# Kernel tuning notes

Measured on AMD Instinct MI355X. Metric: run time of the kernel, lower is better.

The kernel has to match this reference:

```python
import jax, jax.numpy as jnp
import numpy as np

N_NODES = 100000
N_EDGES = 1600000
NFEAT, NHID, NCLASS = 256, 128, 64


def gcn_conv(x, edge_index, edge_weight, W):
    # PyG GCNConv (normalize=False, add_self_loops=False, bias=False):
    # h = x @ W.T; out[i] = sum over edges (j->i) of w_e * h[j]
    h = x @ W.T                                   # [N, out]
    src, dst = edge_index[0], edge_index[1]
    msgs = h[src] * edge_weight[:, None]          # [E, out]
    return jax.ops.segment_sum(msgs, dst, num_segments=x.shape[0])


def setup_inputs() -> dict:
    key = jax.random.key(0)
    ks = jax.random.split(key, 7)
    x = jax.random.normal(ks[0], (N_NODES, NFEAT), dtype=jnp.float32)
    edge_index1 = jax.random.randint(ks[1], (2, N_EDGES), 0, N_NODES, dtype=jnp.int64)
    edge_index2 = jax.random.randint(ks[2], (2, N_EDGES), 0, N_NODES, dtype=jnp.int64)
    edge_weight1 = jax.random.uniform(ks[3], (N_EDGES,), dtype=jnp.float32)
    edge_weight2 = jax.random.uniform(ks[4], (N_EDGES,), dtype=jnp.float32)
    W1 = jax.random.normal(ks[5], (NHID, NFEAT), dtype=jnp.float32) * (1.0 / np.sqrt(NFEAT))
    W2 = jax.random.normal(ks[6], (NCLASS, NHID), dtype=jnp.float32) * (1.0 / np.sqrt(NHID))
    return {"x": x, "edge_index1": edge_index1, "edge_index2": edge_index2,
            "edge_weight1": edge_weight1, "edge_weight2": edge_weight2,
            "W1": W1, "W2": W2}


def reference(x, edge_index1, edge_index2, edge_weight1, edge_weight2, W1, W2):
    h = jax.nn.relu(gcn_conv(x, edge_index1, edge_weight1, W1))
    out = gcn_conv(h, edge_index2, edge_weight2, W2)
    return out
```

## Files before the change

kernel.cpp:

```cpp
#include <hip/hip_runtime.h>

typedef __attribute__((ext_vector_type(8))) short short8;
typedef __attribute__((ext_vector_type(4))) float floatx4;

#define BKT_SHIFT 8
#define BKT_MASK 255
#define SORT_CAP 6144

__device__ __forceinline__ ushort f2bf(float f) {
    uint u = __builtin_bit_cast(uint, f);
    uint r = (u + 0x7FFFu + ((u >> 16) & 1u)) >> 16;
    return (ushort)r;
}
__device__ __forceinline__ float bf2f(ushort u) {
    return __builtin_bit_cast(float, (uint)u << 16);
}

__global__ void detect_i64(const uint* __restrict__ p, int* __restrict__ flag) {
    uint v = p[2 * threadIdx.x + 1];
    unsigned long long b = __ballot(v != 0u);
    if (threadIdx.x == 0) *flag = (b == 0ull) ? 1 : 0;
}

__global__ __launch_bounds__(256) void cvt_w(const float* __restrict__ W1,
                                             const float* __restrict__ W2,
                                             ushort* __restrict__ w1b,
                                             ushort* __restrict__ w2b, int n1, int n2) {
    int i = blockIdx.x * 256 + threadIdx.x;
    if (i < n1) w1b[i] = f2bf(W1[i]);
    else if (i < n1 + n2) w2b[i - n1] = f2bf(W2[i - n1]);
}

template<int K, int NOUT, bool XF32>
__global__ __launch_bounds__(256) void gemm_bt(const void* __restrict__ Xv,
                                               const ushort* __restrict__ W,
                                               ushort* __restrict__ Y, int N) {
    constexpr int NT = NOUT / 16;
    constexpr int KS = K / 32;
    constexpr int ROWS = 64;
    constexpr int RB = XF32 ? K * 4 : K * 2;
    __shared__ __align__(16) char xs[ROWS * RB];

    const int tid  = threadIdx.x;
    const int lane = tid & 63;
    const int wv   = tid >> 6;
    const int t    = lane & 15;
    const int q    = lane >> 4;
    const int rbase = blockIdx.x * ROWS;

    if (XF32) {
        #pragma unroll
        for (int i = 0; i < 16; i++) {
            int rl = wv * 16 + i;
            int grow = rbase + rl;
            if (grow < N) {
                const char* src = (const char*)Xv + (long)grow * RB
                                + ((lane * 16) ^ ((rl & 7) << 5));
                __builtin_amdgcn_global_load_lds(
                    (const __attribute__((address_space(1))) void*)src,
                    (__attribute__((address_space(3))) void*)&xs[rl * RB], 16, 0, 0);
            }
        }
    } else {
        #pragma unroll
        for (int i = 0; i < 4; i++) {
            int rl0 = wv * 16 + i * 4;
            int grow0 = rbase + rl0;
            if (grow0 < N) {
                int rl = rl0 + (lane >> 4);
                const char* src = (const char*)Xv + (long)grow0 * RB + (lane >> 4) * RB
                                + (((lane & 15) * 16) ^ ((rl & 7) << 5));
                __builtin_amdgcn_global_load_lds(
                    (const __attribute__((address_space(1))) void*)src,
                    (__attribute__((address_space(3))) void*)&xs[rl0 * RB], 16, 0, 0);
            }
        }
    }
    __syncthreads();

    floatx4 acc[NT];
    #pragma unroll
    for (int b = 0; b < NT; b++)
        #pragma unroll
        for (int i = 0; i < 4; i++) acc[b][i] = 0.f;

    const int lrow = wv * 16 + t;
    const char* xrow = &xs[lrow * RB];
    const uint swz = (uint)((t & 7) << 5);

    for (int ks = 0; ks < KS; ks++) {
        short8 af;
        if (XF32) {
            uint off = ((uint)(ks * 128 + q * 32)) ^ swz;
            floatx4 lo = *(const floatx4*)(xrow + off);
            floatx4 hi = *(const floatx4*)(xrow + off + 16);
            #pragma unroll
            for (int j = 0; j < 4; j++) {
                af[j]     = (short)f2bf(lo[j]);
                af[4 + j] = (short)f2bf(hi[j]);
            }
        } else {
            uint off = ((uint)(ks * 64 + q * 16)) ^ swz;
            af = *(const short8*)(xrow + off);
        }
        #pragma unroll
        for (int nt = 0; nt < NT; nt++) {
            short8 bf = *(const short8*)(W + (long)(nt * 16 + t) * K + ks * 32 + q * 8);
            acc[nt] = __builtin_amdgcn_mfma_f32_16x16x32_bf16(af, bf, acc[nt], 0, 0, 0);
        }
    }

    const int obase = rbase + wv * 16;
    #pragma unroll
    for (int j = 0; j < 4; j++) {
        int orow = obase + q * 4 + j;
        if (orow < N) {
            #pragma unroll
            for (int nt = 0; nt < NT; nt++)
                Y[(long)orow * NOUT + nt * 16 + t] = f2bf(acc[nt][j]);
        }
    }
}

__global__ __launch_bounds__(256) void bucket_hist(const void* __restrict__ eidx,
                                                   int* __restrict__ bhist, int E, int nbk,
                                                   const int* __restrict__ flag) {
    __shared__ int lc[512];
    for (int t = threadIdx.x; t < 512; t += 256) lc[t] = 0;
    __syncthreads();
    int S = (E + gridDim.x - 1) / gridDim.x;
    int s = blockIdx.x * S, e = min(E, s + S);
    bool f = *flag;
    for (int i = s + threadIdx.x; i < e; i += 256) {
        int dst = f ? (int)((const long long*)eidx)[i + E] : ((const int*)eidx)[i + E];
        atomicAdd(&lc[dst >> BKT_SHIFT], 1);
    }
    __syncthreads();
    for (int t = threadIdx.x; t < nbk; t += 256)
        if (lc[t]) atomicAdd(&bhist[t], lc[t]);
}

__global__ __launch_bounds__(512) void bucket_scan(const int* __restrict__ bhist,
                                                   int* __restrict__ segstart,
                                                   int* __restrict__ cursor, int nbk, int E) {
    __shared__ int s[512];
    int t = threadIdx.x;
    s[t] = (t < nbk) ? bhist[t] : 0;
    __syncthreads();
    for (int off = 1; off < 512; off <<= 1) {
        int v = (t >= off) ? s[t - off] : 0;
        __syncthreads();
        s[t] += v;
        __syncthreads();
    }
    int ex = t ? s[t - 1] : 0;
    if (t < nbk) { segstart[t] = ex; cursor[t] = ex; }
    if (t == 0) segstart[nbk] = E;
}

__global__ __launch_bounds__(256) void bin_edges(const void* __restrict__ eidx,
                                                 const float* __restrict__ ew,
                                                 int* __restrict__ cursor,
                                                 int2* __restrict__ binA, int E, int nbk,
                                                 const int* __restrict__ flag) {
    __shared__ int lc[512], lb[512], lo[512];
    for (int t = threadIdx.x; t < 512; t += 256) { lc[t] = 0; lo[t] = 0; }
    __syncthreads();
    int S = (E + gridDim.x - 1) / gridDim.x;
    int s = blockIdx.x * S, e = min(E, s + S);
    bool f = *flag;
    for (int i = s + threadIdx.x; i < e; i += 256) {
        int dst = f ? (int)((const long long*)eidx)[i + E] : ((const int*)eidx)[i + E];
        atomicAdd(&lc[dst >> BKT_SHIFT], 1);
    }
    __syncthreads();
    for (int t = threadIdx.x; t < nbk; t += 256)
        lb[t] = lc[t] ? atomicAdd(&cursor[t], lc[t]) : 0;
    __syncthreads();
    for (int i = s + threadIdx.x; i < e; i += 256) {
        int src, dst;
        if (f) { const long long* p = (const long long*)eidx; src = (int)p[i]; dst = (int)p[i + E]; }
        else   { const int* p = (const int*)eidx;             src = p[i];      dst = p[i + E]; }
        int bk = dst >> BKT_SHIFT;
        int off = atomicAdd(&lo[bk], 1);
        binA[lb[bk] + off] = make_int2(src | ((dst & BKT_MASK) << 24),
                                       __builtin_bit_cast(int, ew[i]));
    }
}

__global__ __launch_bounds__(256) void sort_bucket(const int2* __restrict__ binA,
                                                   const int* __restrict__ segstart,
                                                   int2* __restrict__ pairs,
                                                   int* __restrict__ rowptr,
                                                   int N, int E, int nbk) {
    __shared__ int cnt[256], cur[256];
    __shared__ int2 ps[SORT_CAP];
    int b = blockIdx.x, t = threadIdx.x;
    int s = segstart[b], e = segstart[b + 1];
    int n = e - s;
    cnt[t] = 0; cur[t] = 0;
    __syncthreads();
    for (int i = s + t; i < e; i += 256)
        atomicAdd(&cnt[(uint)binA[i].x >> 24], 1);
    __syncthreads();
    for (int off = 1; off < 256; off <<= 1) {
        int v = (t >= off) ? cnt[t - off] : 0;
        __syncthreads();
        cnt[t] += v;
        __syncthreads();
    }
    int node = (b << BKT_SHIFT) + t;
    int ex = t ? cnt[t - 1] : 0;
    if (node < N) rowptr[node] = s + ex;
    if (node == N || (b == nbk - 1 && t == 255)) rowptr[N] = E;
    __syncthreads();
    if (n <= SORT_CAP) {
        for (int i = s + t; i < e; i += 256) {
            int2 p = binA[i];
            int dl = (uint)p.x >> 24;
            int pos = (dl ? cnt[dl - 1] : 0) + atomicAdd(&cur[dl], 1);
            ps[pos] = make_int2(p.x & 0x00FFFFFF, p.y);
        }
        __syncthreads();
        for (int j = t; j < n; j += 256) pairs[s + j] = ps[j];
    } else {
        for (int i = s + t; i < e; i += 256) {
            int2 p = binA[i];
            int dl = (uint)p.x >> 24;
            int pos = s + (dl ? cnt[dl - 1] : 0) + atomicAdd(&cur[dl], 1);
            pairs[pos] = make_int2(p.x & 0x00FFFFFF, p.y);
        }
    }
}

template<int F, bool RELU, bool BF16OUT>
__global__ __launch_bounds__(256) void gather_nodes(const ushort* __restrict__ H,
                                                    const int2* __restrict__ pairs,
                                                    const int* __restrict__ rowptr,
                                                    void* __restrict__ out, int N) {
    constexpr int L = F / 2;
    constexpr int NPW = 64 / L;
    int wave = (blockIdx.x * 256 + threadIdx.x) >> 6;
    int lane = threadIdx.x & 63;
    int node = wave * NPW + lane / L;
    int c = lane % L;
    if (node >= N) return;
    int s = rowptr[node], e = rowptr[node + 1];
    float a0 = 0.f, a1 = 0.f, b0 = 0.f, b1 = 0.f;
    float c0 = 0.f, c1 = 0.f, d0 = 0.f, d1 = 0.f;
    for (int i = s; i < e; i += 4) {
        int i1 = min(i + 1, e - 1), i2 = min(i + 2, e - 1), i3 = min(i + 3, e - 1);
        int2 p0 = pairs[i];
        int2 p1 = pairs[i1];
        int2 p2 = pairs[i2];
        int2 p3 = pairs[i3];
        uint h0 = *(const uint*)(H + (long)p0.x * F + 2 * c);
        uint h1 = *(const uint*)(H + (long)p1.x * F + 2 * c);
        uint h2 = *(const uint*)(H + (long)p2.x * F + 2 * c);
        uint h3 = *(const uint*)(H + (long)p3.x * F + 2 * c);
        float w0 = __builtin_bit_cast(float, p0.y);
        float w1 = (i + 1 < e) ? __builtin_bit_cast(float, p1.y) : 0.f;
        float w2 = (i + 2 < e) ? __builtin_bit_cast(float, p2.y) : 0.f;
        float w3 = (i + 3 < e) ? __builtin_bit_cast(float, p3.y) : 0.f;
        a0 += w0 * bf2f((ushort)(h0 & 0xffffu));  a1 += w0 * bf2f((ushort)(h0 >> 16));
        b0 += w1 * bf2f((ushort)(h1 & 0xffffu));  b1 += w1 * bf2f((ushort)(h1 >> 16));
        c0 += w2 * bf2f((ushort)(h2 & 0xffffu));  c1 += w2 * bf2f((ushort)(h2 >> 16));
        d0 += w3 * bf2f((ushort)(h3 & 0xffffu));  d1 += w3 * bf2f((ushort)(h3 >> 16));
    }
    float r0 = (a0 + b0) + (c0 + d0);
    float r1 = (a1 + b1) + (c1 + d1);
    if (BF16OUT) {
        if (RELU) { r0 = fmaxf(r0, 0.f); r1 = fmaxf(r1, 0.f); }
        uint packed = (uint)f2bf(r0) | ((uint)f2bf(r1) << 16);
        ((uint*)out)[(long)node * L + c] = packed;
    } else {
        float2 r; r.x = r0; r.y = r1;
        ((float2*)out)[(long)node * L + c] = r;
    }
}

extern "C" void kernel_launch(void* const* d_in, const int* in_sizes, int n_in,
                              void* d_out, int out_size, void* d_ws, size_t ws_size,
                              hipStream_t stream) {
    const float* x   = (const float*)d_in[0];
    const void*  ei1 = d_in[1];
    const void*  ei2 = d_in[2];
    const float* ew1 = (const float*)d_in[3];
    const float* ew2 = (const float*)d_in[4];
    const float* W1  = (const float*)d_in[5];
    const float* W2  = (const float*)d_in[6];

    const int N = in_sizes[0] / 256;
    const int E = in_sizes[3];
    const int NBK = (N + 255) >> 8;

    char* ws = (char*)d_ws;
    size_t off = 0;
    ushort* XW     = (ushort*)(ws + off); off += (size_t)N * 128 * 2;
    char*   hbufrg = ws + off;            off += (size_t)N * 128 * 2;
    int2*   pairs  = (int2*)  (ws + off); off += (size_t)E * 8;
    int*    rowptr = (int*)   (ws + off); off += (size_t)(N + 1) * 4;
    int*    bhist  = (int*)   (ws + off); off += 512 * 4;
    int*    segst  = (int*)   (ws + off); off += 513 * 4;
    int*    cursor = (int*)   (ws + off); off += 513 * 4;
    ushort* w1b    = (ushort*)(ws + off); off += 128 * 256 * 2;
    ushort* w2b    = (ushort*)(ws + off); off += 64 * 128 * 2;
    int*    flag   = (int*)   (ws + off);
    ushort* hbuf   = (ushort*)hbufrg;
    int2*   binA   = (int2*)hbufrg;
    ushort* H2     = XW;

    detect_i64<<<1, 64, 0, stream>>>((const uint*)ei1, flag);
    cvt_w<<<(128 * 256 + 64 * 128 + 255) / 256, 256, 0, stream>>>(
        W1, W2, w1b, w2b, 128 * 256, 64 * 128);

    int gblocks = (N + 63) / 64;
    gemm_bt<256, 128, true><<<gblocks, 256, 0, stream>>>(x, w1b, XW, N);

    hipMemsetAsync(bhist, 0, 512 * 4, stream);
    bucket_hist<<<256, 256, 0, stream>>>(ei1, bhist, E, NBK, flag);
    bucket_scan<<<1, 512, 0, stream>>>(bhist, segst, cursor, NBK, E);
    bin_edges<<<256, 256, 0, stream>>>(ei1, ew1, cursor, binA, E, NBK, flag);
    sort_bucket<<<NBK, 256, 0, stream>>>(binA, segst, pairs, rowptr, N, E, NBK);
    gather_nodes<128, true, true><<<(N + 3) / 4, 256, 0, stream>>>(
        XW, pairs, rowptr, hbuf, N);

    gemm_bt<128, 64, false><<<gblocks, 256, 0, stream>>>(hbuf, w2b, H2, N);
    hipMemsetAsync(bhist, 0, 512 * 4, stream);
    bucket_hist<<<256, 256, 0, stream>>>(ei2, bhist, E, NBK, flag);
    bucket_scan<<<1, 512, 0, stream>>>(bhist, segst, cursor, NBK, E);
    bin_edges<<<256, 256, 0, stream>>>(ei2, ew2, cursor, binA, E, NBK, flag);
    sort_bucket<<<NBK, 256, 0, stream>>>(binA, segst, pairs, rowptr, N, E, NBK);
    gather_nodes<64, false, false><<<(N * 2 + 7) / 8, 256, 0, stream>>>(
        H2, pairs, rowptr, (float*)d_out, N);
}
```

Baseline: 539.1 us.

## Pre-convert x to bf16, merge prep kernels, separate bin buffer, drop memset

Adds a standalone kernel that converts x from fp32 to bf16, so the first GEMM loads half as many bytes into LDS and no longer converts inside the MFMA loop. The index-width detection and weight conversion are merged into one prep kernel, and bucket_scan now clears the histogram so the second memset is removed. binA gets its own workspace region instead of aliasing hbuf, which uses more workspace memory. The first GEMM is also moved after the histogram and scan launches. The extra conversion pass adds a full read of x plus a bf16 write and read-back, about 100 MB of traffic, which may offset the savings.

```diff
diff --git a/kernel.cpp b/kernel.cpp
--- a/kernel.cpp
+++ b/kernel.cpp
@@ -16,29 +16,49 @@
     return __builtin_bit_cast(float, (uint)u << 16);
 }
 
-__global__ void detect_i64(const uint* __restrict__ p, int* __restrict__ flag) {
-    uint v = p[2 * threadIdx.x + 1];
-    unsigned long long b = __ballot(v != 0u);
-    if (threadIdx.x == 0) *flag = (b == 0ull) ? 1 : 0;
-}
-
-__global__ __launch_bounds__(256) void cvt_w(const float* __restrict__ W1,
-                                             const float* __restrict__ W2,
-                                             ushort* __restrict__ w1b,
-                                             ushort* __restrict__ w2b, int n1, int n2) {
+__global__ __launch_bounds__(256) void prep(const uint* __restrict__ ei,
+                                            int* __restrict__ flag,
+                                            const float* __restrict__ W1,
+                                            const float* __restrict__ W2,
+                                            ushort* __restrict__ w1b,
+                                            ushort* __restrict__ w2b, int n1, int n2) {
+    if (blockIdx.x == 0 && threadIdx.x < 64) {
+        uint v = ei[2 * threadIdx.x + 1];
+        unsigned long long b = __ballot(v != 0u);
+        if (threadIdx.x == 0) *flag = (b == 0ull) ? 1 : 0;
+    }
     int i = blockIdx.x * 256 + threadIdx.x;
     if (i < n1) w1b[i] = f2bf(W1[i]);
     else if (i < n1 + n2) w2b[i - n1] = f2bf(W2[i - n1]);
 }
 
-template<int K, int NOUT, bool XF32>
-__global__ __launch_bounds__(256) void gemm_bt(const void* __restrict__ Xv,
+__global__ __launch_bounds__(256) void cvt_x(const float* __restrict__ X,
+                                             ushort* __restrict__ XB, long n) {
+    long i = ((long)blockIdx.x * 256 + threadIdx.x) * 8;
+    if (i < n) {
+        floatx4 a = *(const floatx4*)(X + i);
+        floatx4 b = *(const floatx4*)(X + i + 4);
+        short8 o;
+        #pragma unroll
+        for (int j = 0; j < 4; j++) {
+            o[j]     = (short)f2bf(a[j]);
+            o[4 + j] = (short)f2bf(b[j]);
+        }
+        *(short8*)(XB + i) = o;
+    }
+}
+
+template<int K, int NOUT>
+__global__ __launch_bounds__(256) void gemm_bt(const ushort* __restrict__ Xb,
                                                const ushort* __restrict__ W,
                                                ushort* __restrict__ Y, int N) {
     constexpr int NT = NOUT / 16;
     constexpr int KS = K / 32;
     constexpr int ROWS = 64;
-    constexpr int RB = XF32 ? K * 4 : K * 2;
+    constexpr int RB = K * 2;
+    constexpr int LPR = RB / 16;
+    constexpr int RPI = 64 / LPR;
+    constexpr int NI = 16 / RPI;
     __shared__ __align__(16) char xs[ROWS * RB];
 
     const int tid  = threadIdx.x;
@@ -48,32 +68,17 @@
     const int q    = lane >> 4;
     const int rbase = blockIdx.x * ROWS;
 
-    if (XF32) {
-        #pragma unroll
-        for (int i = 0; i < 16; i++) {
-            int rl = wv * 16 + i;
-            int grow = rbase + rl;
-            if (grow < N) {
-                const char* src = (const char*)Xv + (long)grow * RB
-                                + ((lane * 16) ^ ((rl & 7) << 5));
-                __builtin_amdgcn_global_load_lds(
-                    (const __attribute__((address_space(1))) void*)src,
-                    (__attribute__((address_space(3))) void*)&xs[rl * RB], 16, 0, 0);
-            }
-        }
-    } else {
-        #pragma unroll
-        for (int i = 0; i < 4; i++) {
-            int rl0 = wv * 16 + i * 4;
-            int grow0 = rbase + rl0;
-            if (grow0 < N) {
-                int rl = rl0 + (lane >> 4);
-                const char* src = (const char*)Xv + (long)grow0 * RB + (lane >> 4) * RB
-                                + (((lane & 15) * 16) ^ ((rl & 7) << 5));
-                __builtin_amdgcn_global_load_lds(
-                    (const __attribute__((address_space(1))) void*)src,
-                    (__attribute__((address_space(3))) void*)&xs[rl0 * RB], 16, 0, 0);
-            }
+    #pragma unroll
+    for (int i = 0; i < NI; i++) {
+        int rl0 = wv * 16 + i * RPI;
+        int grow0 = rbase + rl0;
+        if (grow0 < N) {
+            int rl = rl0 + lane / LPR;
+            const char* src = (const char*)Xb + (long)grow0 * RB + (lane / LPR) * RB
+                            + (((lane % LPR) * 16) ^ ((rl & 7) << 5));
+            __builtin_amdgcn_global_load_lds(
+                (const __attribute__((address_space(1))) void*)src,
+                (__attribute__((address_space(3))) void*)&xs[rl0 * RB], 16, 0, 0);
         }
     }
     __syncthreads();
@@ -89,20 +94,7 @@
     const uint swz = (uint)((t & 7) << 5);
 
     for (int ks = 0; ks < KS; ks++) {
-        short8 af;
-        if (XF32) {
-            uint off = ((uint)(ks * 128 + q * 32)) ^ swz;
-            floatx4 lo = *(const floatx4*)(xrow + off);
-            floatx4 hi = *(const floatx4*)(xrow + off + 16);
-            #pragma unroll
-            for (int j = 0; j < 4; j++) {
-                af[j]     = (short)f2bf(lo[j]);
-                af[4 + j] = (short)f2bf(hi[j]);
-            }
-        } else {
-            uint off = ((uint)(ks * 64 + q * 16)) ^ swz;
-            af = *(const short8*)(xrow + off);
-        }
+        short8 af = *(const short8*)(xrow + (((uint)(ks * 64 + q * 16)) ^ swz));
         #pragma unroll
         for (int nt = 0; nt < NT; nt++) {
             short8 bf = *(const short8*)(W + (long)(nt * 16 + t) * K + ks * 32 + q * 8);
@@ -140,7 +132,7 @@
         if (lc[t]) atomicAdd(&bhist[t], lc[t]);
 }
 
-__global__ __launch_bounds__(512) void bucket_scan(const int* __restrict__ bhist,
+__global__ __launch_bounds__(512) void bucket_scan(int* __restrict__ bhist,
                                                    int* __restrict__ segstart,
                                                    int* __restrict__ cursor, int nbk, int E) {
     __shared__ int s[512];
@@ -154,7 +146,7 @@
         __syncthreads();
     }
     int ex = t ? s[t - 1] : 0;
-    if (t < nbk) { segstart[t] = ex; cursor[t] = ex; }
+    if (t < nbk) { segstart[t] = ex; cursor[t] = ex; bhist[t] = 0; }
     if (t == 0) segstart[nbk] = E;
 }
 
@@ -297,7 +289,8 @@
     char* ws = (char*)d_ws;
     size_t off = 0;
     ushort* XW     = (ushort*)(ws + off); off += (size_t)N * 128 * 2;
-    char*   hbufrg = ws + off;            off += (size_t)N * 128 * 2;
+    ushort* hbuf   = (ushort*)(ws + off); off += (size_t)N * 128 * 2;
+    int2*   binA   = (int2*)  (ws + off); off += (size_t)E * 8;
     int2*   pairs  = (int2*)  (ws + off); off += (size_t)E * 8;
     int*    rowptr = (int*)   (ws + off); off += (size_t)(N + 1) * 4;
     int*    bhist  = (int*)   (ws + off); off += 512 * 4;
@@ -306,27 +299,26 @@
     ushort* w1b    = (ushort*)(ws + off); off += 128 * 256 * 2;
     ushort* w2b    = (ushort*)(ws + off); off += 64 * 128 * 2;
     int*    flag   = (int*)   (ws + off);
-    ushort* hbuf   = (ushort*)hbufrg;
-    int2*   binA   = (int2*)hbufrg;
+    ushort* XB     = hbuf;
     ushort* H2     = XW;
 
-    detect_i64<<<1, 64, 0, stream>>>((const uint*)ei1, flag);
-    cvt_w<<<(128 * 256 + 64 * 128 + 255) / 256, 256, 0, stream>>>(
-        W1, W2, w1b, w2b, 128 * 256, 64 * 128);
-
-    int gblocks = (N + 63) / 64;
-    gemm_bt<256, 128, true><<<gblocks, 256, 0, stream>>>(x, w1b, XW, N);
+    prep<<<160, 256, 0, stream>>>((const uint*)ei1, flag, W1, W2, w1b, w2b,
+                                  128 * 256, 64 * 128);
+    cvt_x<<<(int)(((long)N * 256 / 8 + 255) / 256), 256, 0, stream>>>(x, XB, (long)N * 256);
 
     hipMemsetAsync(bhist, 0, 512 * 4, stream);
     bucket_hist<<<256, 256, 0, stream>>>(ei1, bhist, E, NBK, flag);
     bucket_scan<<<1, 512, 0, stream>>>(bhist, segst, cursor, NBK, E);
+
+    int gblocks = (N + 63) / 64;
+    gemm_bt<256, 128><<<gblocks, 256, 0, stream>>>(XB, w1b, XW, N);
+
     bin_edges<<<256, 256, 0, stream>>>(ei1, ew1, cursor, binA, E, NBK, flag);
     sort_bucket<<<NBK, 256, 0, stream>>>(binA, segst, pairs, rowptr, N, E, NBK);
     gather_nodes<128, true, true><<<(N + 3) / 4, 256, 0, stream>>>(
         XW, pairs, rowptr, hbuf, N);
 
-    gemm_bt<128, 64, false><<<gblocks, 256, 0, stream>>>(hbuf, w2b, H2, N);
-    hipMemsetAsync(bhist, 0, 512 * 4, stream);
+    gemm_bt<128, 64><<<gblocks, 256, 0, stream>>>(hbuf, w2b, H2, N);
     bucket_hist<<<256, 256, 0, stream>>>(ei2, bhist, E, NBK, flag);
     bucket_scan<<<1, 512, 0, stream>>>(bhist, segst, cursor, NBK, E);
     bin_edges<<<256, 256, 0, stream>>>(ei2, ew2, cursor, binA, E, NBK, flag);
```

Measured after the change: 545.4 us. About the same (+1.2%).
